# Performance work log

Measured on AMD Instinct MI355X. Metric: run time of the kernel, lower is better.

The kernel has to match this reference:

```python
import jax, jax.numpy as jnp
import numpy as np

TAU = 0.5  # config.tau
EPS = 1e-12  # F.normalize eps


def _pair_idx(n_i, hi):
    # all pairs (i, j) with i in [0, n_i), j in (i, hi)
    ii, jj = [], []
    for i in range(n_i):
        js = np.arange(i + 1, hi)
        ii.append(np.full(js.shape, i))
        jj.append(js)
    return np.concatenate(ii), np.concatenate(jj)


def setup_inputs() -> dict:
    key = jax.random.key(0)
    ks = jax.random.split(key, 7)
    B, D, H = 512, 768, 256
    s = 0.02
    return {
        "emb_in": jax.random.normal(ks[0], (B, D), jnp.float32),
        "W1": jax.random.normal(ks[1], (H, 2 * D), jnp.float32) * s,
        "b1": jax.random.normal(ks[2], (H,), jnp.float32) * s,
        "W2": jax.random.normal(ks[3], (H, H), jnp.float32) * s,
        "b2": jax.random.normal(ks[4], (H,), jnp.float32) * s,
        "W3": jax.random.normal(ks[5], (1, H), jnp.float32) * s,
        "b3": jax.random.normal(ks[6], (1,), jnp.float32) * s,
    }


def reference(emb_in, W1, b1, W2, b2, W3, b3):
    B, D = emb_in.shape
    n = B // 4
    m = B // 2

    # L2 normalize rows (torch F.normalize)
    z = emb_in / jnp.maximum(jnp.linalg.norm(emb_in, axis=1, keepdims=True), EPS)
    # cosine similarity matrix [B, B]
    S = z @ z.T

    # ---- ContrastiveLoss (NT-Xent style over first n rows) ----
    logits = S / jnp.asarray(TAU, emb_in.dtype)
    not_diag = 1.0 - jnp.eye(B, dtype=emb_in.dtype)
    denom = jnp.sum(not_diag * jnp.exp(logits), axis=1)  # sum_{k != i} exp(S[i,k]/T)
    log_denom = jnp.log(denom)  # [B]
    ci, cj = _pair_idx(n, n)  # pairs i < j < n
    # loss_ij = -log( exp(S[i,j]/T) / denom_i ) = log_denom[i] - logits[i, j]
    closs_sum = jnp.sum(log_denom[ci] - logits[ci, cj])
    closs = (-2.0 * (n - 1) / n) * closs_sum

    # ---- en_loss: pairwise concat + tiny MLP + BCEWithLogits ----
    ei_np, ej_np = _pair_idx(n, B)  # pairs i in [0,n), j in (i, B)
    ei = jnp.asarray(ei_np)
    ej = jnp.asarray(ej_np)
    labels = (ej_np < m).astype(np.float32)  # first m-(i+1) pairs per i are positives
    labels = jnp.asarray(labels)

    x = jnp.concatenate([z[ei], z[ej]], axis=1)  # [P, 2D]
    h1 = jax.nn.relu(x @ W1.T + b1)              # [P, H]
    h2 = jax.nn.relu(h1 @ W2.T + b2)             # [P, H]
    logit = (h2 @ W3.T + b3)[:, 0]               # [P]

    # BCEWithLogitsLoss (mean), numerically stable form
    bce = jnp.maximum(logit, 0.0) - logit * labels + jnp.log1p(jnp.exp(-jnp.abs(logit)))
    eloss = jnp.mean(bce)

    return closs + eloss
```

## Files before the change

kernel.cpp:

```cpp
#include <hip/hip_runtime.h>
#include <hip/hip_bf16.h>
#include <math.h>

#define B 512
#define D 768
#define H 256
#define NN 128
#define MM 256
#define P_PAIRS 57280
#define NPBLK_P 448

typedef _Float16 f16x8 __attribute__((ext_vector_type(8)));
typedef float f32x4 __attribute__((ext_vector_type(4)));


__global__ __launch_bounds__(256) void k_prep(const float* __restrict__ emb,
                                              const float* __restrict__ W1,
                                              const float* __restrict__ W2,
                                              _Float16* __restrict__ zH,
                                              _Float16* __restrict__ W1H,
                                              _Float16* __restrict__ W2H) {
    __shared__ float invs[8];
    int bx = blockIdx.x;
    int tid = threadIdx.x;
    int w = tid >> 6, lane = tid & 63;

    if (bx < 64) {
        int g8 = bx;
        int grp = g8 >> 1;
        int h = g8 & 1;
        #pragma unroll
        for (int rr = 0; rr < 2; rr++) {
            int r8 = 2 * w + rr;
            const float* rp = emb + (8 * g8 + r8) * D;
            float ss = 0.f;
            #pragma unroll
            for (int it = 0; it < 12; it++) {
                float v = rp[lane + 64 * it];
                ss += v * v;
            }
            #pragma unroll
            for (int m = 1; m <= 32; m <<= 1) ss += __shfl_xor(ss, m);
            if (lane == 0) invs[r8] = 1.0f / fmaxf(sqrtf(ss), 1e-12f);
        }
        __syncthreads();
        #pragma unroll
        for (int it = 0; it < 3; it++) {
            int chunk = it * 256 + tid;
            int s = chunk >> 5;
            int x = chunk & 31;
            int q = x >> 3, r8 = x & 7;
            int r = h * 8 + r8;
            const float* src = emb + (8 * g8 + r8) * D + 32 * s + 8 * q;
            float inv = invs[r8];
            float4 a = *(const float4*)src;
            float4 bb = *(const float4*)(src + 4);
            f16x8 o;
            o[0] = (_Float16)(a.x * inv); o[1] = (_Float16)(a.y * inv);
            o[2] = (_Float16)(a.z * inv); o[3] = (_Float16)(a.w * inv);
            o[4] = (_Float16)(bb.x * inv); o[5] = (_Float16)(bb.y * inv);
            o[6] = (_Float16)(bb.z * inv); o[7] = (_Float16)(bb.w * inv);
            *(f16x8*)(zH + ((grp * 24 + s) * 64 + q * 16 + r) * 8) = o;
        }
    } else if (bx < 128) {
        int g = (bx - 64) >> 1;
        int sh = (bx - 64) & 1;
        #pragma unroll
        for (int it = 0; it < 3; it++) {
            int chunk = it * 256 + tid;
            int s = sh * 12 + (chunk >> 6);
            int lc = chunk & 63;
            int q = lc >> 4, r = lc & 15;
            int n = 16 * g + r;
            const float* src = W1 + (n & 255) * (2 * D) + (n >> 8) * D + 32 * s + 8 * q;
            float4 a = *(const float4*)src;
            float4 bb = *(const float4*)(src + 4);
            f16x8 o;
            o[0] = (_Float16)a.x; o[1] = (_Float16)a.y; o[2] = (_Float16)a.z; o[3] = (_Float16)a.w;
            o[4] = (_Float16)bb.x; o[5] = (_Float16)bb.y; o[6] = (_Float16)bb.z; o[7] = (_Float16)bb.w;
            *(f16x8*)(W1H + ((g * 24 + s) * 64 + lc) * 8) = o;
        }
    } else {
        int g = (bx - 128) >> 1;
        int sh = (bx - 128) & 1;
        int s = sh * 4 + (tid >> 6);
        int lc = tid & 63;
        int q = lc >> 4, r = lc & 15;
        const float* src = W2 + (16 * g + r) * H + 32 * s + 8 * q;
        float4 a = *(const float4*)src;
        float4 bb = *(const float4*)(src + 4);
        f16x8 o;
        o[0] = (_Float16)a.x; o[1] = (_Float16)a.y; o[2] = (_Float16)a.z; o[3] = (_Float16)a.w;
        o[4] = (_Float16)bb.x; o[5] = (_Float16)bb.y; o[6] = (_Float16)bb.z; o[7] = (_Float16)bb.w;
        *(f16x8*)(W2H + ((g * 8 + s) * 64 + lc) * 8) = o;
    }
}

__global__ __launch_bounds__(128) void k_uv(const _Float16* __restrict__ zH,
                                            const _Float16* __restrict__ W1H,
                                            const float* __restrict__ b1,
                                            _Float16* __restrict__ Up,
                                            _Float16* __restrict__ Vv) {
    int w = threadIdx.x >> 6;
    int lane = threadIdx.x & 63;
    int r = lane & 15, q = lane >> 4;
    int gid = blockIdx.x * 2 + w;
    int gm = gid >> 4;
    int gnp = gid & 15;

    f32x4 acc[2] = {};
    #pragma unroll 4
    for (int s = 0; s < 24; s++) {
        f16x8 a = *(const f16x8*)(zH + ((gm * 24 + s) * 64 + lane) * 8);
        #pragma unroll
        for (int nt = 0; nt < 2; nt++) {
            f16x8 bb = *(const f16x8*)(W1H + (((gnp * 2 + nt) * 24 + s) * 64 + lane) * 8);
            acc[nt] = __builtin_amdgcn_mfma_f32_16x16x32_f16(a, bb, acc[nt], 0, 0, 0);
        }
    }
    #pragma unroll
    for (int nt = 0; nt < 2; nt++) {
        int n = (gnp * 2 + nt) * 16 + r;
        float bias = (n < H) ? b1[n] : 0.f;
        #pragma unroll
        for (int rr = 0; rr < 4; rr++) {
            int m = gm * 16 + 4 * q + rr;
            float C = acc[nt][rr] + bias;
            if (n < H) Up[m * H + n] = (_Float16)C;
            else       Vv[m * H + (n - H)] = (_Float16)C;
        }
    }
}

__global__ __launch_bounds__(256, 2) void k_pairs(const _Float16* __restrict__ Up,
                                                  const _Float16* __restrict__ Vv,
                                                  const _Float16* __restrict__ W2H,
                                                  const _Float16* __restrict__ zH,
                                                  const float* __restrict__ b2,
                                                  const float* __restrict__ W3,
                                                  const float* __restrict__ b3,
                                                  float* __restrict__ bcepart,
                                                  float* __restrict__ esp,
                                                  float* __restrict__ slp) {
    int tid = threadIdx.x;
    int w = tid >> 6, lane = tid & 63;
    int r = lane & 15, q = lane >> 4;
    int bx = blockIdx.x;

    if (bx >= NPBLK_P) {
        int t = (bx - NPBLK_P) * 4 + w;
        int gm = t >> 3;
        int slot = t & 7;
        int gn0 = slot * 4;
        f32x4 acc[4] = {};
        #pragma unroll 4
        for (int s = 0; s < 24; s++) {
            f16x8 a = *(const f16x8*)(zH + ((gm * 24 + s) * 64 + lane) * 8);
            #pragma unroll
            for (int nt = 0; nt < 4; nt++) {
                f16x8 bb = *(const f16x8*)(zH + (((gn0 + nt) * 24 + s) * 64 + lane) * 8);
                acc[nt] = __builtin_amdgcn_mfma_f32_16x16x32_f16(a, bb, acc[nt], 0, 0, 0);
            }
        }
        #pragma unroll
        for (int rr = 0; rr < 4; rr++) {
            int irow = gm * 16 + q * 4 + rr;
            float es = 0.f, sl = 0.f;
            #pragma unroll
            for (int nt = 0; nt < 4; nt++) {
                int kcol = (gn0 + nt) * 16 + r;
                float C = acc[nt][rr];
                if (kcol != irow) es += expf(2.f * C);
                if (kcol > irow && kcol < NN) sl += 2.f * C;
            }
            #pragma unroll
            for (int m = 1; m <= 8; m <<= 1) {
                es += __shfl_xor(es, m);
                sl += __shfl_xor(sl, m);
            }
            if (r == 0) {
                esp[slot * NN + irow] = es;
                slp[slot * NN + irow] = sl;
            }
        }
        return;
    }

    __shared__ _Float16 h1[128][264];
    __shared__ float redbuf[4][128];
    __shared__ float red2[2];

    int p0 = bx * 128;

    #pragma unroll
    for (int uu = 0; uu < 2; uu++) {
        int u = uu * 256 + tid;
        int row = u >> 2, cq = u & 3;
        int p = p0 + row;
        if (p >= P_PAIRS) p = P_PAIRS - 1;
        float disc = 1046529.f - 8.f * (float)p;
        int i = (int)((1023.f - sqrtf(disc)) * 0.5f);
        if (i < 0) i = 0;
        if (i > NN - 1) i = NN - 1;
        while (i > 0 && i * (1023 - i) / 2 > p) i--;
        while ((i + 1) * (1022 - i) / 2 <= p) i++;
        int j = i + 1 + (p - i * (1023 - i) / 2);

        const _Float16* up = Up + i * H + 64 * cq;
        const _Float16* vp = Vv + j * H + 64 * cq;
        #pragma unroll
        for (int c8 = 0; c8 < 8; c8++) {
            f16x8 u8 = *(const f16x8*)(up + 8 * c8);
            f16x8 v8 = *(const f16x8*)(vp + 8 * c8);
            f16x8 zero = {};
            f16x8 hv = __builtin_elementwise_max(u8 + v8, zero);
            *(f16x8*)&h1[row][64 * cq + 8 * c8] = hv;
        }
    }
    __syncthreads();

    f32x4 acc[8][4] = {};
    #pragma unroll
    for (int s = 0; s < 8; s++) {
        f16x8 bb[4];
        #pragma unroll
        for (int nt = 0; nt < 4; nt++)
            bb[nt] = *(const f16x8*)(W2H + (((4 * w + nt) * 8 + s) * 64 + lane) * 8);
        #pragma unroll
        for (int mt = 0; mt < 8; mt++) {
            f16x8 a = *(const f16x8*)&h1[16 * mt + r][32 * s + 8 * q];
            #pragma unroll
            for (int nt = 0; nt < 4; nt++)
                acc[mt][nt] = __builtin_amdgcn_mfma_f32_16x16x32_f16(a, bb[nt], acc[mt][nt], 0, 0, 0);
        }
    }

    float b2v[4], w3v[4];
    #pragma unroll
    for (int nt = 0; nt < 4; nt++) {
        int n = 64 * w + 16 * nt + r;
        b2v[nt] = b2[n];
        w3v[nt] = W3[n];
    }
    #pragma unroll
    for (int mt = 0; mt < 8; mt++) {
        float part[4] = {0.f, 0.f, 0.f, 0.f};
        #pragma unroll
        for (int nt = 0; nt < 4; nt++)
            #pragma unroll
            for (int rr = 0; rr < 4; rr++) {
                float h2 = fmaxf(acc[mt][nt][rr] + b2v[nt], 0.f);
                part[rr] += h2 * w3v[nt];
            }
        #pragma unroll
        for (int rr = 0; rr < 4; rr++) {
            float v = part[rr];
            #pragma unroll
            for (int m = 1; m <= 8; m <<= 1) v += __shfl_xor(v, m);
            if (r == 0) redbuf[w][16 * mt + 4 * q + rr] = v;
        }
    }
    __syncthreads();

    if (tid < 128) {
        int p = p0 + tid;
        float lsum = 0.f;
        if (p < P_PAIRS) {
            float disc = 1046529.f - 8.f * (float)p;
            int i = (int)((1023.f - sqrtf(disc)) * 0.5f);
            if (i < 0) i = 0;
            if (i > NN - 1) i = NN - 1;
            while (i > 0 && i * (1023 - i) / 2 > p) i--;
            while ((i + 1) * (1022 - i) / 2 <= p) i++;
            int j = i + 1 + (p - i * (1023 - i) / 2);

            float logit = redbuf[0][tid] + redbuf[1][tid] +
                          redbuf[2][tid] + redbuf[3][tid] + b3[0];
            float label = (j < MM) ? 1.f : 0.f;
            lsum = fmaxf(logit, 0.f) - logit * label + log1pf(expf(-fabsf(logit)));
        }
        #pragma unroll
        for (int off = 32; off > 0; off >>= 1) lsum += __shfl_down(lsum, off);
        if ((tid & 63) == 0) red2[tid >> 6] = lsum;
    }
    __syncthreads();
    if (tid == 0) bcepart[bx] = red2[0] + red2[1];
}

__global__ __launch_bounds__(256) void k_final(const float* __restrict__ esp,
                                               const float* __restrict__ slp,
                                               const float* __restrict__ bcepart,
                                               float* __restrict__ out) {
    __shared__ float red[256];
    int t = threadIdx.x;

    float s = 0.f;
    for (int p = t; p < NPBLK_P; p += 256) s += bcepart[p];
    red[t] = s;
    __syncthreads();
    for (int st = 128; st > 0; st >>= 1) {
        if (t < st) red[t] += red[t + st];
        __syncthreads();
    }
    float bce_total = red[0];
    __syncthreads();

    float v = 0.f;
    if (t < NN) {
        float es = 0.f, sl = 0.f;
        #pragma unroll
        for (int s8 = 0; s8 < 8; s8++) {
            es += esp[s8 * NN + t];
            sl += slp[s8 * NN + t];
        }
        v = (float)(NN - 1 - t) * logf(es) - sl;
    }
    red[t] = v;
    __syncthreads();
    for (int st = 128; st > 0; st >>= 1) {
        if (t < st) red[t] += red[t + st];
        __syncthreads();
    }
    if (t == 0) {
        float closs = (-2.0f * (float)(NN - 1) / (float)NN) * red[0];
        out[0] = closs + bce_total / (float)P_PAIRS;
    }
}

extern "C" void kernel_launch(void* const* d_in, const int* in_sizes, int n_in,
                              void* d_out, int out_size, void* d_ws, size_t ws_size,
                              hipStream_t stream) {
    const float* emb = (const float*)d_in[0];
    const float* W1  = (const float*)d_in[1];
    const float* b1  = (const float*)d_in[2];
    const float* W2  = (const float*)d_in[3];
    const float* b2  = (const float*)d_in[4];
    const float* W3  = (const float*)d_in[5];
    const float* b3  = (const float*)d_in[6];
    float* out = (float*)d_out;

    float* ws = (float*)d_ws;
    float* esp     = ws;
    float* slp     = ws + 1024;
    float* bcepart = ws + 2048;
    _Float16* zH  = (_Float16*)(ws + 3072);
    _Float16* W1H = zH + B * D;
    _Float16* W2H = W1H + 2 * H * D;
    _Float16* Up  = W2H + H * H;
    _Float16* Vv  = Up + B * H;

    k_prep<<<160, 256, 0, stream>>>(emb, W1, W2, zH, W1H, W2H);
    k_uv<<<256, 128, 0, stream>>>(zH, W1H, b1, Up, Vv);
    k_pairs<<<NPBLK_P + 16, 256, 0, stream>>>(Up, Vv, W2H, zH, b2, W3, b3,
                                              bcepart, esp, slp);
    k_final<<<1, 256, 0, stream>>>(esp, slp, bcepart, out);
}
```

Measured before the change: 99.18 us.

## Fuse prep and U/V GEMM into one kernel, converting fp32 inputs inline

Merges the conversion kernel and the U/V projection GEMM into a single launch. The GEMM blocks now read fp32 emb and W1 directly, recompute row norms, and convert to fp16 in registers, so the W1H staging buffer and one kernel launch go away. The cost is that each GEMM block redundantly recomputes norms and re-reads fp32 data with a less coalesced strided access pattern, while zH and W2H are still produced by other blocks of the same launch.

```diff
diff --git a/kernel.cpp b/kernel.cpp
--- a/kernel.cpp
+++ b/kernel.cpp
@@ -14,13 +14,33 @@
 typedef float f32x4 __attribute__((ext_vector_type(4)));
 
 
-__global__ __launch_bounds__(256) void k_prep(const float* __restrict__ emb,
-                                              const float* __restrict__ W1,
-                                              const float* __restrict__ W2,
-                                              _Float16* __restrict__ zH,
-                                              _Float16* __restrict__ W1H,
-                                              _Float16* __restrict__ W2H) {
-    __shared__ float invs[8];
+__device__ __forceinline__ f16x8 cvt8s(float4 a, float4 b, float sc) {
+    f16x8 o;
+    o[0] = (_Float16)(a.x * sc); o[1] = (_Float16)(a.y * sc);
+    o[2] = (_Float16)(a.z * sc); o[3] = (_Float16)(a.w * sc);
+    o[4] = (_Float16)(b.x * sc); o[5] = (_Float16)(b.y * sc);
+    o[6] = (_Float16)(b.z * sc); o[7] = (_Float16)(b.w * sc);
+    return o;
+}
+
+__device__ __forceinline__ f16x8 cvt8(float4 a, float4 b) {
+    f16x8 o;
+    o[0] = (_Float16)a.x; o[1] = (_Float16)a.y;
+    o[2] = (_Float16)a.z; o[3] = (_Float16)a.w;
+    o[4] = (_Float16)b.x; o[5] = (_Float16)b.y;
+    o[6] = (_Float16)b.z; o[7] = (_Float16)b.w;
+    return o;
+}
+
+__global__ __launch_bounds__(256) void k_prep_uv(const float* __restrict__ emb,
+                                                 const float* __restrict__ W1,
+                                                 const float* __restrict__ W2,
+                                                 const float* __restrict__ b1,
+                                                 _Float16* __restrict__ zH,
+                                                 _Float16* __restrict__ W2H,
+                                                 _Float16* __restrict__ Up,
+                                                 _Float16* __restrict__ Vv) {
+    __shared__ float invs[16];
     int bx = blockIdx.x;
     int tid = threadIdx.x;
     int w = tid >> 6, lane = tid & 63;
@@ -55,79 +75,74 @@
             float inv = invs[r8];
             float4 a = *(const float4*)src;
             float4 bb = *(const float4*)(src + 4);
-            f16x8 o;
-            o[0] = (_Float16)(a.x * inv); o[1] = (_Float16)(a.y * inv);
-            o[2] = (_Float16)(a.z * inv); o[3] = (_Float16)(a.w * inv);
-            o[4] = (_Float16)(bb.x * inv); o[5] = (_Float16)(bb.y * inv);
-            o[6] = (_Float16)(bb.z * inv); o[7] = (_Float16)(bb.w * inv);
-            *(f16x8*)(zH + ((grp * 24 + s) * 64 + q * 16 + r) * 8) = o;
-        }
-    } else if (bx < 128) {
+            *(f16x8*)(zH + ((grp * 24 + s) * 64 + q * 16 + r) * 8) = cvt8s(a, bb, inv);
+        }
+    } else if (bx < 96) {
         int g = (bx - 64) >> 1;
         int sh = (bx - 64) & 1;
-        #pragma unroll
-        for (int it = 0; it < 3; it++) {
-            int chunk = it * 256 + tid;
-            int s = sh * 12 + (chunk >> 6);
-            int lc = chunk & 63;
-            int q = lc >> 4, r = lc & 15;
-            int n = 16 * g + r;
-            const float* src = W1 + (n & 255) * (2 * D) + (n >> 8) * D + 32 * s + 8 * q;
-            float4 a = *(const float4*)src;
-            float4 bb = *(const float4*)(src + 4);
-            f16x8 o;
-            o[0] = (_Float16)a.x; o[1] = (_Float16)a.y; o[2] = (_Float16)a.z; o[3] = (_Float16)a.w;
-            o[4] = (_Float16)bb.x; o[5] = (_Float16)bb.y; o[6] = (_Float16)bb.z; o[7] = (_Float16)bb.w;
-            *(f16x8*)(W1H + ((g * 24 + s) * 64 + lc) * 8) = o;
-        }
-    } else {
-        int g = (bx - 128) >> 1;
-        int sh = (bx - 128) & 1;
         int s = sh * 4 + (tid >> 6);
         int lc = tid & 63;
         int q = lc >> 4, r = lc & 15;
         const float* src = W2 + (16 * g + r) * H + 32 * s + 8 * q;
         float4 a = *(const float4*)src;
         float4 bb = *(const float4*)(src + 4);
-        f16x8 o;
-        o[0] = (_Float16)a.x; o[1] = (_Float16)a.y; o[2] = (_Float16)a.z; o[3] = (_Float16)a.w;
-        o[4] = (_Float16)bb.x; o[5] = (_Float16)bb.y; o[6] = (_Float16)bb.z; o[7] = (_Float16)bb.w;
-        *(f16x8*)(W2H + ((g * 8 + s) * 64 + lc) * 8) = o;
-    }
-}
-
-__global__ __launch_bounds__(128) void k_uv(const _Float16* __restrict__ zH,
-                                            const _Float16* __restrict__ W1H,
-                                            const float* __restrict__ b1,
-                                            _Float16* __restrict__ Up,
-                                            _Float16* __restrict__ Vv) {
-    int w = threadIdx.x >> 6;
-    int lane = threadIdx.x & 63;
-    int r = lane & 15, q = lane >> 4;
-    int gid = blockIdx.x * 2 + w;
-    int gm = gid >> 4;
-    int gnp = gid & 15;
-
-    f32x4 acc[2] = {};
-    #pragma unroll 4
-    for (int s = 0; s < 24; s++) {
-        f16x8 a = *(const f16x8*)(zH + ((gm * 24 + s) * 64 + lane) * 8);
+        *(f16x8*)(W2H + ((g * 8 + s) * 64 + lc) * 8) = cvt8(a, bb);
+    } else {
+        int gblk = bx - 96;
+        int gm = gblk >> 2;
+        int gnp = (gblk & 3) * 4 + w;
+
+        #pragma unroll
+        for (int rr = 0; rr < 4; rr++) {
+            int r16 = 4 * w + rr;
+            const float* rp = emb + (gm * 16 + r16) * D;
+            float ss = 0.f;
+            #pragma unroll
+            for (int it = 0; it < 12; it++) {
+                float v = rp[lane + 64 * it];
+                ss += v * v;
+            }
+            #pragma unroll
+            for (int m = 1; m <= 32; m <<= 1) ss += __shfl_xor(ss, m);
+            if (lane == 0) invs[r16] = 1.0f / fmaxf(sqrtf(ss), 1e-12f);
+        }
+        __syncthreads();
+
+        int r = lane & 15, q = lane >> 4;
+        float inv = invs[r];
+        const float* arow = emb + (gm * 16 + r) * D + 8 * q;
+        const float* brow[2];
         #pragma unroll
         for (int nt = 0; nt < 2; nt++) {
-            f16x8 bb = *(const f16x8*)(W1H + (((gnp * 2 + nt) * 24 + s) * 64 + lane) * 8);
-            acc[nt] = __builtin_amdgcn_mfma_f32_16x16x32_f16(a, bb, acc[nt], 0, 0, 0);
-        }
-    }
-    #pragma unroll
-    for (int nt = 0; nt < 2; nt++) {
-        int n = (gnp * 2 + nt) * 16 + r;
-        float bias = (n < H) ? b1[n] : 0.f;
-        #pragma unroll
-        for (int rr = 0; rr < 4; rr++) {
-            int m = gm * 16 + 4 * q + rr;
-            float C = acc[nt][rr] + bias;
-            if (n < H) Up[m * H + n] = (_Float16)C;
-            else       Vv[m * H + (n - H)] = (_Float16)C;
+            int n = (gnp * 2 + nt) * 16 + r;
+            brow[nt] = W1 + (n & 255) * (2 * D) + (n >> 8) * D + 8 * q;
+        }
+
+        f32x4 acc[2] = {};
+        #pragma unroll 4
+        for (int s = 0; s < 24; s++) {
+            float4 a0 = *(const float4*)(arow + 32 * s);
+            float4 a1 = *(const float4*)(arow + 32 * s + 4);
+            f16x8 a = cvt8s(a0, a1, inv);
+            #pragma unroll
+            for (int nt = 0; nt < 2; nt++) {
+                float4 b0 = *(const float4*)(brow[nt] + 32 * s);
+                float4 b1v = *(const float4*)(brow[nt] + 32 * s + 4);
+                f16x8 bb = cvt8(b0, b1v);
+                acc[nt] = __builtin_amdgcn_mfma_f32_16x16x32_f16(a, bb, acc[nt], 0, 0, 0);
+            }
+        }
+        #pragma unroll
+        for (int nt = 0; nt < 2; nt++) {
+            int n = (gnp * 2 + nt) * 16 + r;
+            float bias = (n < H) ? b1[n] : 0.f;
+            #pragma unroll
+            for (int rr = 0; rr < 4; rr++) {
+                int m = gm * 16 + 4 * q + rr;
+                float C = acc[nt][rr] + bias;
+                if (n < H) Up[m * H + n] = (_Float16)C;
+                else       Vv[m * H + (n - H)] = (_Float16)C;
+            }
         }
     }
 }
@@ -344,13 +359,11 @@
     float* slp     = ws + 1024;
     float* bcepart = ws + 2048;
     _Float16* zH  = (_Float16*)(ws + 3072);
-    _Float16* W1H = zH + B * D;
-    _Float16* W2H = W1H + 2 * H * D;
+    _Float16* W2H = zH + B * D;
     _Float16* Up  = W2H + H * H;
     _Float16* Vv  = Up + B * H;
 
-    k_prep<<<160, 256, 0, stream>>>(emb, W1, W2, zH, W1H, W2H);
-    k_uv<<<256, 128, 0, stream>>>(zH, W1H, b1, Up, Vv);
+    k_prep_uv<<<224, 256, 0, stream>>>(emb, W1, W2, b1, zH, W2H, Up, Vv);
     k_pairs<<<NPBLK_P + 16, 256, 0, stream>>>(Up, Vv, W2H, zH, b2, W3, b3,
                                               bcepart, esp, slp);
     k_final<<<1, 256, 0, stream>>>(esp, slp, bcepart, out);
```

Result: slower. 110.2 us (+11.1%).
